# Kernel tuning notes

Hardware: AMD Instinct MI355X
Metric: run time of the kernel (lower is better)

Reference implementation:

```python
import jax, jax.numpy as jnp
import numpy as np

N, E, F_IN, H, C, N_CLS = 50000, 800000, 128, 4, 32, 10
NEG_SLOPE = 0.2


def setup_inputs() -> dict:
    key = jax.random.key(0)
    ks = jax.random.split(key, 24)
    d = {}
    d["x"] = jax.random.normal(ks[0], (N, F_IN), jnp.float32)
    d["edge_index"] = jax.random.randint(ks[1], (2, E), 0, N, jnp.int32)

    def lin(k, fan_in, shape):
        return jax.random.normal(k, shape, jnp.float32) / np.float32(np.sqrt(fan_in))

    # conv1: F_IN -> H*C, heads H, concat
    d["W1"]  = lin(ks[2], F_IN, (F_IN, H * C))
    d["a1s"] = lin(ks[3], C, (H, C))
    d["a1d"] = lin(ks[4], C, (H, C))
    d["b1"]  = jnp.zeros((H * C,), jnp.float32)
    d["lin1_W"] = lin(ks[5], F_IN, (F_IN, H * C))
    d["lin1_b"] = jnp.zeros((H * C,), jnp.float32)
    # conv2: H*C -> H*C
    d["W2"]  = lin(ks[6], H * C, (H * C, H * C))
    d["a2s"] = lin(ks[7], C, (H, C))
    d["a2d"] = lin(ks[8], C, (H, C))
    d["b2"]  = jnp.zeros((H * C,), jnp.float32)
    d["lin2_W"] = lin(ks[9], H * C, (H * C, H * C))
    d["lin2_b"] = jnp.zeros((H * C,), jnp.float32)
    # conv3: H*C -> N_CLS, heads H, concat=False (mean over heads)
    d["W3"]  = lin(ks[10], H * C, (H * C, H * N_CLS))
    d["a3s"] = lin(ks[11], N_CLS, (H, N_CLS))
    d["a3d"] = lin(ks[12], N_CLS, (H, N_CLS))
    d["b3"]  = jnp.zeros((N_CLS,), jnp.float32)
    d["lin3_W"] = lin(ks[13], H * C, (H * C, N_CLS))
    d["lin3_b"] = jnp.zeros((N_CLS,), jnp.float32)
    return d


def gat_conv(x, src, dst, W, a_s, a_d, b, heads, out_ch, concat):
    n = x.shape[0]
    h = (x @ W).reshape(n, heads, out_ch)                # [N,H,C]
    alpha_src = jnp.sum(h * a_s, axis=-1)                # [N,H]
    alpha_dst = jnp.sum(h * a_d, axis=-1)                # [N,H]
    e = jax.nn.leaky_relu(alpha_src[src] + alpha_dst[dst], NEG_SLOPE)  # [E,H]
    # segment softmax over edges grouped by destination node
    m = jax.ops.segment_max(e, dst, num_segments=n)      # [N,H]
    p = jnp.exp(e - m[dst])
    denom = jax.ops.segment_sum(p, dst, num_segments=n)  # [N,H]
    alpha = p / (denom[dst] + 1e-16)                     # [E,H]
    out = jax.ops.segment_sum(alpha[:, :, None] * h[src], dst, num_segments=n)  # [N,H,C]
    out = out.reshape(n, heads * out_ch) if concat else out.mean(axis=1)
    return out + b


def reference(x, edge_index, W1, a1s, a1d, b1, lin1_W, lin1_b,
              W2, a2s, a2d, b2, lin2_W, lin2_b,
              W3, a3s, a3d, b3, lin3_W, lin3_b):
    n = x.shape[0]
    # PyG GATConv adds self-loops by default
    loops = jnp.arange(n, dtype=edge_index.dtype)
    src = jnp.concatenate([edge_index[0], loops])
    dst = jnp.concatenate([edge_index[1], loops])

    x = jax.nn.elu(gat_conv(x, src, dst, W1, a1s, a1d, b1, H, C, True) + x @ lin1_W + lin1_b)
    x = jax.nn.elu(gat_conv(x, src, dst, W2, a2s, a2d, b2, H, C, True) + x @ lin2_W + lin2_b)
    x = gat_conv(x, src, dst, W3, a3s, a3d, b3, H, N_CLS, False) + x @ lin3_W + lin3_b
    return x
```

## Files before the change

kernel.cpp:

```cpp
#include <hip/hip_runtime.h>
#include <math.h>


#define HEADS 4
#define FILLB 4096
#define FILL_U 4

typedef __attribute__((ext_vector_type(8))) short short8v;
typedef __attribute__((ext_vector_type(4))) float float4v;

__device__ __forceinline__ float lrelu(float v) { return v > 0.f ? v : 0.2f * v; }

__device__ __forceinline__ unsigned short f2bf(float f) {
    unsigned u = __float_as_uint(f);
    unsigned r = u + 0x7FFFu + ((u >> 16) & 1u);
    return (unsigned short)(r >> 16);
}
__device__ __forceinline__ float bf2f(unsigned short u) {
    return __uint_as_float(((unsigned)u) << 16);
}

__device__ void castX_body(const float* __restrict__ x, unsigned short* __restrict__ xb,
                           int n4, int i) {
    if (i >= n4) return;
    float4 v = *(const float4*)&x[(size_t)i * 4];
    ushort4 o;
    o.x = f2bf(v.x); o.y = f2bf(v.y); o.z = f2bf(v.z); o.w = f2bf(v.w);
    *(ushort4*)&xb[(size_t)i * 4] = o;
}

__device__ void hist_body(const int* __restrict__ dst, int E, int* __restrict__ deg, int t) {
    int e = t * 4;
    if (e + 3 < E) {
        int4 d = *(const int4*)&dst[e];
        atomicAdd(&deg[d.x], 1);
        atomicAdd(&deg[d.y], 1);
        atomicAdd(&deg[d.z], 1);
        atomicAdd(&deg[d.w], 1);
    } else {
        for (; e < E; ++e) atomicAdd(&deg[dst[e]], 1);
    }
}

__device__ void packB12_body(const float* __restrict__ W, const float* __restrict__ LW,
                             const float* __restrict__ a_s, const float* __restrict__ a_d,
                             unsigned short* __restrict__ BT, int i) {
    if (i >= 320 * 128) return;
    int m = i >> 7, k = i & 127;
    float v = 0.f;
    if (m < 128) {
        v = W[(size_t)k * 128 + m];
    } else if (m < 256) {
        v = LW[(size_t)k * 128 + (m - 128)];
    } else if (m < 260) {
        int h = m - 256;
        for (int c = 0; c < 32; ++c)
            v = fmaf(W[(size_t)k * 128 + h * 32 + c], a_s[h * 32 + c], v);
    } else if (m < 264) {
        int h = m - 260;
        for (int c = 0; c < 32; ++c)
            v = fmaf(W[(size_t)k * 128 + h * 32 + c], a_d[h * 32 + c], v);
    }
    BT[i] = f2bf(v);
}

__device__ void packB3_body(const float* __restrict__ W3, const float* __restrict__ LW3,
                            const float* __restrict__ a_s, const float* __restrict__ a_d,
                            unsigned short* __restrict__ BT, int i) {
    if (i >= 128 * 128) return;
    int m = i >> 7, k = i & 127;
    float v = 0.f;
    if (m < 40) {
        v = W3[(size_t)k * 40 + m];
    } else if (m < 50) {
        v = LW3[(size_t)k * 10 + (m - 40)];
    } else if (m >= 64 && m < 68) {
        int h = m - 64;
        for (int c = 0; c < 10; ++c)
            v = fmaf(W3[(size_t)k * 40 + h * 10 + c], a_s[h * 10 + c], v);
    } else if (m >= 68 && m < 72) {
        int h = m - 68;
        for (int c = 0; c < 10; ++c)
            v = fmaf(W3[(size_t)k * 40 + h * 10 + c], a_d[h * 10 + c], v);
    }
    BT[i] = f2bf(v);
}

__device__ void gemm_body(const unsigned short* __restrict__ A,
                          const unsigned short* __restrict__ BT,
                          unsigned short* __restrict__ C,
                          float* __restrict__ asrc, float* __restrict__ adst,
                          int nrows, int Mc, int Cstride, int permStore, int bidx) {
    const int wave = threadIdx.x >> 6;
    const int lane = threadIdx.x & 63;
    const int row0 = bidx * 64 + wave * 16;
    const int lrow = lane & 15;
    const int kgrp = lane >> 4;

    int arow = row0 + lrow;
    if (arow >= nrows) arow = nrows - 1;
    const unsigned short* Ap = A + (size_t)arow * 128 + kgrp * 8;

    short8v afrag[4];
#pragma unroll
    for (int t = 0; t < 4; ++t) afrag[t] = *(const short8v*)(Ap + t * 32);

    const int nDataBlk = Mc >> 6;
    for (int cb = 0; cb < nDataBlk; ++cb) {
        const unsigned short* Bp = BT + (size_t)(cb * 64 + lrow) * 128 + kgrp * 8;
        float4v acc[4] = {{0.f,0.f,0.f,0.f},{0.f,0.f,0.f,0.f},{0.f,0.f,0.f,0.f},{0.f,0.f,0.f,0.f}};
#pragma unroll
        for (int t = 0; t < 4; ++t) {
#pragma unroll
            for (int kk = 0; kk < 4; ++kk) {
                short8v b = *(const short8v*)(Bp + kk * 16 * 128 + t * 32);
                acc[kk] = __builtin_amdgcn_mfma_f32_16x16x32_bf16(afrag[t], b, acc[kk], 0, 0, 0);
            }
        }
#pragma unroll
        for (int r = 0; r < 4; ++r) {
            int row = row0 + kgrp * 4 + r;
            if (row >= nrows) continue;
            if (!permStore) {
                size_t base = (size_t)row * Cstride + cb * 64 + lrow;
                C[base]      = f2bf(acc[0][r]);
                C[base + 16] = f2bf(acc[1][r]);
                C[base + 32] = f2bf(acc[2][r]);
                C[base + 48] = f2bf(acc[3][r]);
            } else {
#pragma unroll
                for (int kk = 0; kk < 4; ++kk) {
                    int col = lrow + kk * 16;
                    int pos;
                    if (col < 40)      pos = (col / 5) * 8 + (col % 5);
                    else if (col < 50) pos = 64 + (col - 40);
                    else continue;
                    C[(size_t)row * 80 + pos] = f2bf(acc[kk][r]);
                }
            }
        }
    }

    {
        const unsigned short* Bp = BT + (size_t)(Mc + lrow) * 128 + kgrp * 8;
        float4v acc0 = {0.f, 0.f, 0.f, 0.f};
#pragma unroll
        for (int t = 0; t < 4; ++t) {
            short8v b = *(const short8v*)(Bp + t * 32);
            acc0 = __builtin_amdgcn_mfma_f32_16x16x32_bf16(afrag[t], b, acc0, 0, 0, 0);
        }
        if (lrow < 8) {
            float* dst = (lrow < 4) ? asrc : adst;
            int hh = lrow & 3;
#pragma unroll
            for (int r = 0; r < 4; ++r) {
                int row = row0 + kgrp * 4 + r;
                if (row < nrows) dst[(size_t)row * 4 + hh] = acc0[r];
            }
        }
    }
}

__device__ void fill_body(const int* __restrict__ ei, int E, int N,
                          const int* __restrict__ rowptr, int* __restrict__ cur,
                          int* __restrict__ adj, int bid) {
    const int bucket = bid & 7;
    const int grp    = bid >> 3;
    const int ngrp   = FILLB >> 3;
    const int npb    = (N + 7) >> 3;
    const int lo = bucket * npb;
    const int hi = (lo + npb < N) ? lo + npb : N;

    for (int i = lo + grp * 256 + (int)threadIdx.x; i < hi; i += ngrp * 256)
        adj[rowptr[i]] = i;

    const int chunkSz = 256 * FILL_U;
    const int nchunks = (E + chunkSz - 1) / chunkSz;
    const int* dstRow = ei + E;
    for (int c = grp; c < nchunks; c += ngrp) {
        int base = c * chunkSz + (int)threadIdx.x;
#pragma unroll
        for (int k = 0; k < FILL_U; ++k) {
            int e = base + k * 256;
            if (e < E) {
                int d = dstRow[e];
                if (d >= lo && d < hi) {
                    int pos = rowptr[d] + 1 + atomicAdd(&cur[d], 1);
                    adj[pos] = ei[e];
                }
            }
        }
    }
}

__global__ __launch_bounds__(256) void prep_fused(
    const float* __restrict__ x, unsigned short* __restrict__ xb, int nCast, int n4,
    const int* __restrict__ ei, int E, int* __restrict__ deg, int nHist,
    const float* __restrict__ W1, const float* __restrict__ l1W,
    const float* __restrict__ a1s, const float* __restrict__ a1d, unsigned short* __restrict__ BT1,
    const float* __restrict__ W2, const float* __restrict__ l2W,
    const float* __restrict__ a2s, const float* __restrict__ a2d, unsigned short* __restrict__ BT2,
    const float* __restrict__ W3, const float* __restrict__ l3W,
    const float* __restrict__ a3s, const float* __restrict__ a3d, unsigned short* __restrict__ BT3)
{
    const int nPack12 = 160;
    int b = blockIdx.x;
    if (b < nCast) {
        castX_body(x, xb, n4, b * 256 + threadIdx.x);
    } else if ((b -= nCast) < nHist) {
        hist_body(ei + E, E, deg, b * 256 + threadIdx.x);
    } else if ((b -= nHist) < nPack12) {
        packB12_body(W1, l1W, a1s, a1d, BT1, b * 256 + threadIdx.x);
    } else if ((b -= nPack12) < nPack12) {
        packB12_body(W2, l2W, a2s, a2d, BT2, b * 256 + threadIdx.x);
    } else {
        b -= nPack12;
        packB3_body(W3, l3W, a3s, a3d, BT3, b * 256 + threadIdx.x);
    }
}

__global__ __launch_bounds__(256) void gemm_fill_fused(
    const unsigned short* __restrict__ A, const unsigned short* __restrict__ BT,
    unsigned short* __restrict__ C, float* __restrict__ asrc, float* __restrict__ adst,
    int nrows, int rowBlocks,
    const int* __restrict__ ei, int E, int N,
    const int* __restrict__ rowptr, int* __restrict__ cur, int* __restrict__ adj)
{
    if ((int)blockIdx.x < rowBlocks)
        gemm_body(A, BT, C, asrc, adst, nrows, 256, 256, 0, blockIdx.x);
    else
        fill_body(ei, E, N, rowptr, cur, adj, blockIdx.x - rowBlocks);
}

__global__ __launch_bounds__(256) void mfma_gemm(const unsigned short* __restrict__ A,
                                                 const unsigned short* __restrict__ BT,
                                                 unsigned short* __restrict__ C,
                                                 float* __restrict__ asrc,
                                                 float* __restrict__ adst,
                                                 int nrows, int Mc, int Cstride,
                                                 int permStore) {
    gemm_body(A, BT, C, asrc, adst, nrows, Mc, Cstride, permStore, blockIdx.x);
}

__global__ void scan_block(const int* __restrict__ in, int* __restrict__ out,
                           int* __restrict__ bsum, int n) {
    __shared__ int tmp[256];
    int i = blockIdx.x * 256 + threadIdx.x;
    int v = (i < n) ? in[i] + 1 : 0;
    tmp[threadIdx.x] = v;
    __syncthreads();
    for (int d = 1; d < 256; d <<= 1) {
        int t = (threadIdx.x >= d) ? tmp[threadIdx.x - d] : 0;
        __syncthreads();
        tmp[threadIdx.x] += t;
        __syncthreads();
    }
    if (i < n) out[i] = tmp[threadIdx.x] - v;
    if (threadIdx.x == 255) bsum[blockIdx.x] = tmp[255];
}

__global__ void scan_bsum(int* bsum, int nb) {
    __shared__ int tmp[256];
    int v = (threadIdx.x < nb) ? bsum[threadIdx.x] : 0;
    tmp[threadIdx.x] = v;
    __syncthreads();
    for (int d = 1; d < 256; d <<= 1) {
        int t = (threadIdx.x >= d) ? tmp[threadIdx.x - d] : 0;
        __syncthreads();
        tmp[threadIdx.x] += t;
        __syncthreads();
    }
    if (threadIdx.x < nb) bsum[threadIdx.x] = tmp[threadIdx.x] - v;
}

__global__ void scan_add(int* out, const int* __restrict__ bsum, int n) {
    int i = blockIdx.x * 256 + threadIdx.x;
    if (i < n) out[i] += bsum[blockIdx.x];
}

__global__ __launch_bounds__(256) void gat_gather128(
    const int* __restrict__ rowptr, const int* __restrict__ adj, int ET,
    const float* __restrict__ asrc, const float* __restrict__ adst,
    const unsigned short* __restrict__ Hb,
    const float* __restrict__ bias, const float* __restrict__ lbias,
    unsigned short* __restrict__ xout, int n)
{
    int node = (blockIdx.x * 256 + threadIdx.x) >> 6;
    int lane = threadIdx.x & 63;
    if (node >= n) return;
    int beg = rowptr[node];
    int end = (node + 1 < n) ? rowptr[node + 1] : ET;

    int ep = lane >> 4;
    int q  = lane & 15;
    int c0 = q * 8;
    int h  = q >> 2;
    float adh = adst[(size_t)node * 4 + h];

    float accp = 0.f;
    float a[8];
#pragma unroll
    for (int k = 0; k < 8; ++k) a[k] = 0.f;

    int j = beg + ep;
    while (j < end) {
        int j1 = j + 4, j2 = j + 8, j3 = j + 12;
        bool v1 = j1 < end, v2 = j2 < end, v3 = j3 < end;
        int s0 = adj[j];
        int s1 = v1 ? adj[j1] : s0;
        int s2 = v2 ? adj[j2] : s0;
        int s3 = v3 ? adj[j3] : s0;
        float av0 = asrc[(size_t)s0 * 4 + h];
        float av1 = asrc[(size_t)s1 * 4 + h];
        float av2 = asrc[(size_t)s2 * 4 + h];
        float av3 = asrc[(size_t)s3 * 4 + h];
        short8v hv0 = *(const short8v*)&Hb[(size_t)s0 * 256 + c0];
        short8v hv1 = *(const short8v*)&Hb[(size_t)s1 * 256 + c0];
        short8v hv2 = *(const short8v*)&Hb[(size_t)s2 * 256 + c0];
        short8v hv3 = *(const short8v*)&Hb[(size_t)s3 * 256 + c0];
        float p0 = __expf(lrelu(av0 + adh));
        float p1 = v1 ? __expf(lrelu(av1 + adh)) : 0.f;
        float p2 = v2 ? __expf(lrelu(av2 + adh)) : 0.f;
        float p3 = v3 ? __expf(lrelu(av3 + adh)) : 0.f;
        accp += (p0 + p1) + (p2 + p3);
#pragma unroll
        for (int k = 0; k < 8; ++k) {
            float t0 = fmaf(p0, bf2f((unsigned short)hv0[k]), a[k]);
            float t1 = fmaf(p1, bf2f((unsigned short)hv1[k]), t0);
            float t2 = fmaf(p2, bf2f((unsigned short)hv2[k]), t1);
            a[k] = fmaf(p3, bf2f((unsigned short)hv3[k]), t2);
        }
        j += 16;
    }
#pragma unroll
    for (int off = 16; off <= 32; off <<= 1) {
        accp += __shfl_xor(accp, off);
#pragma unroll
        for (int k = 0; k < 8; ++k) a[k] += __shfl_xor(a[k], off);
    }

    if (ep == 0) {
        float inv = 1.f / (accp + 1e-16f);
        short8v lv = *(const short8v*)&Hb[(size_t)node * 256 + 128 + c0];
        unsigned short w[8];
#pragma unroll
        for (int k = 0; k < 8; ++k) {
            float v = a[k] * inv + bias[c0 + k] + bf2f((unsigned short)lv[k]) + lbias[c0 + k];
            v = v > 0.f ? v : __expf(v) - 1.f;
            w[k] = f2bf(v);
        }
        *(short8v*)&xout[(size_t)node * 128 + c0] = *(short8v*)w;
    }
}

__global__ __launch_bounds__(256) void gat_gather40(
    const int* __restrict__ rowptr, const int* __restrict__ adj, int ET,
    const float* __restrict__ asrc, const float* __restrict__ adst,
    const unsigned short* __restrict__ Hb3,
    const float* __restrict__ bias, const float* __restrict__ lbias,
    float* __restrict__ out, int n)
{
    int node = (blockIdx.x * 256 + threadIdx.x) >> 6;
    int lane = threadIdx.x & 63;
    if (node >= n) return;
    int beg = rowptr[node];
    int end = (node + 1 < n) ? rowptr[node + 1] : ET;

    int slot = lane >> 3;
    int sub  = lane & 7;
    int h    = sub >> 1;
    float adh = adst[(size_t)node * 4 + h];

    float accp = 0.f;
    float a[5];
#pragma unroll
    for (int k = 0; k < 5; ++k) a[k] = 0.f;

    int j = beg + slot;
    while (j < end) {
        int j1 = j + 8;
        bool v1 = j1 < end;
        int s0 = adj[j];
        int s1 = v1 ? adj[j1] : s0;
        float av0 = asrc[(size_t)s0 * 4 + h];
        float av1 = asrc[(size_t)s1 * 4 + h];
        short8v hv0 = *(const short8v*)&Hb3[(size_t)s0 * 80 + sub * 8];
        short8v hv1 = *(const short8v*)&Hb3[(size_t)s1 * 80 + sub * 8];
        float p0 = __expf(lrelu(av0 + adh));
        float p1 = v1 ? __expf(lrelu(av1 + adh)) : 0.f;
        accp += p0 + p1;
#pragma unroll
        for (int k = 0; k < 5; ++k) {
            float t = fmaf(p0, bf2f((unsigned short)hv0[k]), a[k]);
            a[k] = fmaf(p1, bf2f((unsigned short)hv1[k]), t);
        }
        j += 16;
    }
#pragma unroll
    for (int off = 8; off <= 32; off <<= 1) {
        accp += __shfl_xor(accp, off);
#pragma unroll
        for (int k = 0; k < 5; ++k) a[k] += __shfl_xor(a[k], off);
    }
    float inv = 0.25f / (accp + 1e-16f);
#pragma unroll
    for (int k = 0; k < 5; ++k) a[k] *= inv;
#pragma unroll
    for (int off = 2; off <= 4; off <<= 1) {
#pragma unroll
        for (int k = 0; k < 5; ++k) a[k] += __shfl_xor(a[k], off);
    }

    if (lane < 2) {
        int cc0 = sub * 5;
#pragma unroll
        for (int k = 0; k < 5; ++k) {
            float lin = bf2f(Hb3[(size_t)node * 80 + 64 + cc0 + k]);
            out[(size_t)node * 10 + cc0 + k] = a[k] + bias[cc0 + k] + lin + lbias[cc0 + k];
        }
    }
}

extern "C" void kernel_launch(void* const* d_in, const int* in_sizes, int n_in,
                              void* d_out, int out_size, void* d_ws, size_t ws_size,
                              hipStream_t stream) {
    const float* x   = (const float*)d_in[0];
    const int*   ei  = (const int*)d_in[1];
    const float* W1  = (const float*)d_in[2];
    const float* a1s = (const float*)d_in[3];
    const float* a1d = (const float*)d_in[4];
    const float* b1  = (const float*)d_in[5];
    const float* l1W = (const float*)d_in[6];
    const float* l1b = (const float*)d_in[7];
    const float* W2  = (const float*)d_in[8];
    const float* a2s = (const float*)d_in[9];
    const float* a2d = (const float*)d_in[10];
    const float* b2  = (const float*)d_in[11];
    const float* l2W = (const float*)d_in[12];
    const float* l2b = (const float*)d_in[13];
    const float* W3  = (const float*)d_in[14];
    const float* a3s = (const float*)d_in[15];
    const float* a3d = (const float*)d_in[16];
    const float* b3  = (const float*)d_in[17];
    const float* l3W = (const float*)d_in[18];
    const float* l3b = (const float*)d_in[19];

    const int N  = in_sizes[0] / 128;
    const int E  = in_sizes[1] / 2;
    const int ET = E + N;

    unsigned short* Xb  = (unsigned short*)d_ws;
    unsigned short* Hb  = Xb + (size_t)N * 128;
    unsigned short* BT1 = Hb + (size_t)N * 256;
    unsigned short* BT2 = BT1 + 320 * 128;
    unsigned short* BT3 = BT2 + 320 * 128;
    float* asrc = (float*)(BT3 + 128 * 128);
    float* adst = asrc + (size_t)N * 4;
    int* deg    = (int*)(adst + (size_t)N * 4);
    int* cur    = deg + N;
    int* rowptr = cur + N;
    int* bsum   = rowptr + N;
    int* adj    = bsum + 256;

    const int nScanBlocks = (N + 255) / 256;
    const int waveBlocks  = (N * 64 + 255) / 256;
    const int rowBlocks   = (N + 63) / 64;
    const int nCast = (N * 32 + 255) / 256;
    const int nHist = (E / 4 + 256) / 256;
    const int prepBlocks = nCast + nHist + 160 + 160 + 64;

    hipMemsetAsync(deg, 0, (size_t)N * 2 * 4, stream);
    prep_fused<<<prepBlocks, 256, 0, stream>>>(
        x, Xb, nCast, N * 32, ei, E, deg, nHist,
        W1, l1W, a1s, a1d, BT1, W2, l2W, a2s, a2d, BT2, W3, l3W, a3s, a3d, BT3);
    scan_block<<<nScanBlocks, 256, 0, stream>>>(deg, rowptr, bsum, N);
    scan_bsum<<<1, 256, 0, stream>>>(bsum, nScanBlocks);
    scan_add<<<nScanBlocks, 256, 0, stream>>>(rowptr, bsum, N);

    gemm_fill_fused<<<rowBlocks + FILLB, 256, 0, stream>>>(
        Xb, BT1, Hb, asrc, adst, N, rowBlocks, ei, E, N, rowptr, cur, adj);
    gat_gather128<<<waveBlocks, 256, 0, stream>>>(rowptr, adj, ET, asrc, adst, Hb, b1, l1b, Xb, N);

    mfma_gemm<<<rowBlocks, 256, 0, stream>>>(Xb, BT2, Hb, asrc, adst, N, 256, 256, 0);
    gat_gather128<<<waveBlocks, 256, 0, stream>>>(rowptr, adj, ET, asrc, adst, Hb, b2, l2b, Xb, N);

    mfma_gemm<<<rowBlocks, 256, 0, stream>>>(Xb, BT3, Hb, asrc, adst, N, 64, 80, 1);
    gat_gather40<<<waveBlocks, 256, 0, stream>>>(rowptr, adj, ET, asrc, adst, Hb, b3, l3b, (float*)d_out, N);
}
```

Baseline: 275.8 us.

## Interleave GEMM and fill blocks in fused launch; unroll layer-3 gather by four

The fused GEMM+CSR-fill kernel now spreads GEMM block groups evenly among fill block groups, in groups of 8 that keep the destination-bucket mapping, instead of placing all GEMM blocks first. The aim is to overlap compute-bound MFMA work with atomic-heavy fill work on the same CUs. The final-layer gather loop now processes four edges per slot per iteration instead of two, giving more loads in flight. Fill groups stay at 512, and the grid size now depends on the GEMM group count. Indexing for nGB is subtle: fill group ids are derived from g minus the number of GEMM groups seen so far.

```diff
diff --git a/kernel.cpp b/kernel.cpp
--- a/kernel.cpp
+++ b/kernel.cpp
@@ -3,8 +3,8 @@
 
 
 #define HEADS 4
-#define FILLB 4096
 #define FILL_U 4
+#define NFILLG 512
 
 typedef __attribute__((ext_vector_type(8))) short short8v;
 typedef __attribute__((ext_vector_type(4))) float float4v;
@@ -163,21 +163,18 @@
 
 __device__ void fill_body(const int* __restrict__ ei, int E, int N,
                           const int* __restrict__ rowptr, int* __restrict__ cur,
-                          int* __restrict__ adj, int bid) {
-    const int bucket = bid & 7;
-    const int grp    = bid >> 3;
-    const int ngrp   = FILLB >> 3;
-    const int npb    = (N + 7) >> 3;
+                          int* __restrict__ adj, int grp, int bucket) {
+    const int npb = (N + 7) >> 3;
     const int lo = bucket * npb;
     const int hi = (lo + npb < N) ? lo + npb : N;
 
-    for (int i = lo + grp * 256 + (int)threadIdx.x; i < hi; i += ngrp * 256)
+    for (int i = lo + grp * 256 + (int)threadIdx.x; i < hi; i += NFILLG * 256)
         adj[rowptr[i]] = i;
 
     const int chunkSz = 256 * FILL_U;
     const int nchunks = (E + chunkSz - 1) / chunkSz;
     const int* dstRow = ei + E;
-    for (int c = grp; c < nchunks; c += ngrp) {
+    for (int c = grp; c < nchunks; c += NFILLG) {
         int base = c * chunkSz + (int)threadIdx.x;
 #pragma unroll
         for (int k = 0; k < FILL_U; ++k) {
@@ -222,14 +219,22 @@
 __global__ __launch_bounds__(256) void gemm_fill_fused(
     const unsigned short* __restrict__ A, const unsigned short* __restrict__ BT,
     unsigned short* __restrict__ C, float* __restrict__ asrc, float* __restrict__ adst,
-    int nrows, int rowBlocks,
+    int nrows, int rowBlocks, int GG, int S,
     const int* __restrict__ ei, int E, int N,
     const int* __restrict__ rowptr, int* __restrict__ cur, int* __restrict__ adj)
 {
-    if ((int)blockIdx.x < rowBlocks)
-        gemm_body(A, BT, C, asrc, adst, nrows, 256, 256, 0, blockIdx.x);
-    else
-        fill_body(ei, E, N, rowptr, cur, adj, blockIdx.x - rowBlocks);
+    int g  = blockIdx.x >> 3;
+    int l8 = blockIdx.x & 7;
+    bool isGemm = (g % S == 0) && (g / S < GG);
+    if (isGemm) {
+        int gb = (g / S) * 8 + l8;
+        if (gb < rowBlocks)
+            gemm_body(A, BT, C, asrc, adst, nrows, 256, 256, 0, gb);
+    } else {
+        int nGB = g / S + 1;
+        if (nGB > GG) nGB = GG;
+        fill_body(ei, E, N, rowptr, cur, adj, g - nGB, l8);
+    }
 }
 
 __global__ __launch_bounds__(256) void mfma_gemm(const unsigned short* __restrict__ A,
@@ -378,23 +383,33 @@
 
     int j = beg + slot;
     while (j < end) {
-        int j1 = j + 8;
-        bool v1 = j1 < end;
+        int j1 = j + 8, j2 = j + 16, j3 = j + 24;
+        bool v1 = j1 < end, v2 = j2 < end, v3 = j3 < end;
         int s0 = adj[j];
         int s1 = v1 ? adj[j1] : s0;
+        int s2 = v2 ? adj[j2] : s0;
+        int s3 = v3 ? adj[j3] : s0;
         float av0 = asrc[(size_t)s0 * 4 + h];
         float av1 = asrc[(size_t)s1 * 4 + h];
+        float av2 = asrc[(size_t)s2 * 4 + h];
+        float av3 = asrc[(size_t)s3 * 4 + h];
         short8v hv0 = *(const short8v*)&Hb3[(size_t)s0 * 80 + sub * 8];
         short8v hv1 = *(const short8v*)&Hb3[(size_t)s1 * 80 + sub * 8];
+        short8v hv2 = *(const short8v*)&Hb3[(size_t)s2 * 80 + sub * 8];
+        short8v hv3 = *(const short8v*)&Hb3[(size_t)s3 * 80 + sub * 8];
         float p0 = __expf(lrelu(av0 + adh));
         float p1 = v1 ? __expf(lrelu(av1 + adh)) : 0.f;
-        accp += p0 + p1;
+        float p2 = v2 ? __expf(lrelu(av2 + adh)) : 0.f;
+        float p3 = v3 ? __expf(lrelu(av3 + adh)) : 0.f;
+        accp += (p0 + p1) + (p2 + p3);
 #pragma unroll
         for (int k = 0; k < 5; ++k) {
-            float t = fmaf(p0, bf2f((unsigned short)hv0[k]), a[k]);
-            a[k] = fmaf(p1, bf2f((unsigned short)hv1[k]), t);
-        }
-        j += 16;
+            float t0 = fmaf(p0, bf2f((unsigned short)hv0[k]), a[k]);
+            float t1 = fmaf(p1, bf2f((unsigned short)hv1[k]), t0);
+            float t2 = fmaf(p2, bf2f((unsigned short)hv2[k]), t1);
+            a[k] = fmaf(p3, bf2f((unsigned short)hv3[k]), t2);
+        }
+        j += 32;
     }
 #pragma unroll
     for (int off = 8; off <= 32; off <<= 1) {
@@ -468,6 +483,9 @@
     const int nCast = (N * 32 + 255) / 256;
     const int nHist = (E / 4 + 256) / 256;
     const int prepBlocks = nCast + nHist + 160 + 160 + 64;
+    const int GG = (rowBlocks + 7) / 8;
+    const int Tg = NFILLG + GG;
+    const int S  = Tg / GG;
 
     hipMemsetAsync(deg, 0, (size_t)N * 2 * 4, stream);
     prep_fused<<<prepBlocks, 256, 0, stream>>>(
@@ -477,8 +495,8 @@
     scan_bsum<<<1, 256, 0, stream>>>(bsum, nScanBlocks);
     scan_add<<<nScanBlocks, 256, 0, stream>>>(rowptr, bsum, N);
 
-    gemm_fill_fused<<<rowBlocks + FILLB, 256, 0, stream>>>(
-        Xb, BT1, Hb, asrc, adst, N, rowBlocks, ei, E, N, rowptr, cur, adj);
+    gemm_fill_fused<<<Tg * 8, 256, 0, stream>>>(
+        Xb, BT1, Hb, asrc, adst, N, rowBlocks, GG, S, ei, E, N, rowptr, cur, adj);
     gat_gather128<<<waveBlocks, 256, 0, stream>>>(rowptr, adj, ET, asrc, adst, Hb, b1, l1b, Xb, N);
 
     mfma_gemm<<<rowBlocks, 256, 0, stream>>>(Xb, BT2, Hb, asrc, adst, N, 256, 256, 0);
```

Measured after the change: 299.6 us. 8.6% more time.
